# Kernel optimization log

Hardware: AMD Instinct MI355X
Metric: run time of the kernel (lower is better)

The kernel has to match this reference:

```python
import jax, jax.numpy as jnp
import numpy as np

B, S, D, H = 2, 2048, 2048, 16
DH = D // H
CLIP = 8.0
NEG_INF = float('-inf')


def _layernorm(x, g, b, eps=1e-5):
    m = jnp.mean(x, axis=-1, keepdims=True)
    v = jnp.mean(jnp.square(x - m), axis=-1, keepdims=True)
    return (x - m) * jax.lax.rsqrt(v + eps) * g + b


def setup_inputs() -> dict:
    key = jax.random.key(0)
    ks = jax.random.split(key, 6)
    return {
        'x': jax.random.normal(ks[0], (B, S, D), dtype=jnp.float32),
        'attn_bias': jax.random.normal(ks[1], (1, H, 1, S), dtype=jnp.float32) * 0.1,
        'key_padding_mask': jnp.ones((B, S), dtype=bool),
        'Wqkv_w': jax.random.normal(ks[2], (3 * D, D), dtype=jnp.float32) * 0.02,
        'Wqkv_b': jnp.zeros((3 * D,), dtype=jnp.float32),
        'q_ln_g': jnp.ones((D,), dtype=jnp.float32),
        'q_ln_b': jnp.zeros((D,), dtype=jnp.float32),
        'k_ln_g': jnp.ones((D,), dtype=jnp.float32),
        'k_ln_b': jnp.zeros((D,), dtype=jnp.float32),
        'out_w': jax.random.normal(ks[3], (D, D), dtype=jnp.float32) * 0.02,
        'out_b': jnp.zeros((D,), dtype=jnp.float32),
    }


def reference(x, attn_bias, key_padding_mask, Wqkv_w, Wqkv_b,
              q_ln_g, q_ln_b, k_ln_g, k_ln_b, out_w, out_b):
    # Fused QKV projection + clamp
    qkv = x @ Wqkv_w.T + Wqkv_b                      # [B,S,3D]
    qkv = jnp.clip(qkv, -CLIP, CLIP)
    q, k, v = jnp.split(qkv, 3, axis=-1)             # each [B,S,D]
    # Optional per-projection LayerNorm (attn_qk_ln=True)
    q = _layernorm(q, q_ln_g, q_ln_b)
    k = _layernorm(k, k_ln_g, k_ln_b)
    # Split heads
    q = q.reshape(B, S, H, DH)
    k = k.reshape(B, S, H, DH)
    v = v.reshape(B, S, H, DH)
    scale = 1.0 / np.sqrt(DH)
    scores = jnp.einsum('bqhd,bkhd->bhqk', q, k) * scale  # [B,H,S,S]
    scores = scores + attn_bias
    # key padding mask
    scores = jnp.where(key_padding_mask[:, None, None, :], scores, NEG_INF)
    # causal mask
    causal = jnp.tril(jnp.ones((S, S), dtype=bool))
    scores = jnp.where(causal[None, None, :, :], scores, NEG_INF)
    w = jax.nn.softmax(scores, axis=-1)
    ctx = jnp.einsum('bhqk,bkhd->bqhd', w, v).reshape(B, S, D)
    return ctx @ out_w.T + out_b
```

## Files before the change

kernel.cpp:

```cpp
#include <hip/hip_runtime.h>
#include <math.h>

#define B_   2
#define S_   2048
#define D_   2048
#define H_   16
#define DH_  128
#define ND3  6144
#define MROWS 4096

typedef __bf16 bf16;
typedef __attribute__((ext_vector_type(8))) __bf16 bf16x8;
typedef __attribute__((ext_vector_type(4))) float f32x4;

static constexpr float CLIP_V = 8.0f;
static constexpr float SCALE_V = 0.08838834764831845f;

__device__ __forceinline__ void async_load16(const void* g, void* l) {
    __builtin_amdgcn_global_load_lds(
        (const __attribute__((address_space(1))) void*)g,
        (__attribute__((address_space(3))) void*)l, 16, 0, 0);
}

__global__ __launch_bounds__(256) void cvt_kernel(const float* __restrict__ src,
                                                  bf16* __restrict__ dst, int n4)
{
    int i = blockIdx.x * 256 + threadIdx.x;
    if (i >= n4) return;
    float4 v = ((const float4*)src)[i];
    union { bf16 h[4]; uint2 u; } o;
    o.h[0] = (bf16)v.x; o.h[1] = (bf16)v.y; o.h[2] = (bf16)v.z; o.h[3] = (bf16)v.w;
    ((uint2*)dst)[i] = o.u;
}

template <bool CLAMP, typename OUT_T>
__global__ __launch_bounds__(256) void gemm_mfma(
    const bf16* __restrict__ A, const bf16* __restrict__ Bw,
    const float* __restrict__ bias, OUT_T* __restrict__ C,
    int M, int N, int K)
{
    __shared__ __align__(16) bf16 As[128][64];
    __shared__ __align__(16) bf16 Bs[128][64];

    const int tid  = threadIdx.x;
    const int lane = tid & 63;
    const int w    = tid >> 6;
    const int wr   = w >> 1, wc = w & 1;
    const int l15  = lane & 15, lg = lane >> 4;
    const int m0 = blockIdx.y * 128, n0 = blockIdx.x * 128;

    f32x4 acc[4][4] = {};

    const int srow = lane >> 3;
    const int scol = (lane & 7) * 8;

    for (int k0 = 0; k0 < K; k0 += 64) {
#pragma unroll
        for (int c = 0; c < 4; ++c) {
            int r = (c * 4 + w) * 8 + srow;
            async_load16(A  + (size_t)(m0 + r) * K + k0 + scol,
                         (char*)&As[0][0] + (c * 4 + w) * 1024);
            async_load16(Bw + (size_t)(n0 + r) * K + k0 + scol,
                         (char*)&Bs[0][0] + (c * 4 + w) * 1024);
        }
        __syncthreads();

#pragma unroll
        for (int kk = 0; kk < 2; ++kk) {
            bf16x8 af[4], bfv[4];
#pragma unroll
            for (int i = 0; i < 4; ++i) {
                int ra = wr * 64 + i * 16 + l15;
                af[i]  = *(const bf16x8*)((const char*)&As[0][0] + ra * 128 + kk * 64 + lg * 16);
                int rb = wc * 64 + i * 16 + l15;
                bfv[i] = *(const bf16x8*)((const char*)&Bs[0][0] + rb * 128 + kk * 64 + lg * 16);
            }
#pragma unroll
            for (int i = 0; i < 4; ++i)
#pragma unroll
                for (int j = 0; j < 4; ++j)
                    acc[i][j] = __builtin_amdgcn_mfma_f32_16x16x32_bf16(
                        af[i], bfv[j], acc[i][j], 0, 0, 0);
        }
        __syncthreads();
    }

#pragma unroll
    for (int j = 0; j < 4; ++j) {
        int n = n0 + wc * 64 + j * 16 + l15;
        float bn = bias[n];
#pragma unroll
        for (int i = 0; i < 4; ++i) {
            int mbase = m0 + wr * 64 + i * 16 + lg * 4;
#pragma unroll
            for (int r = 0; r < 4; ++r) {
                float v = acc[i][j][r] + bn;
                if (CLAMP) v = fminf(fmaxf(v, -CLIP_V), CLIP_V);
                if constexpr (sizeof(OUT_T) == 2)
                    C[(size_t)(mbase + r) * N + n] = (OUT_T)v;
                else
                    C[(size_t)(mbase + r) * N + n] = v;
            }
        }
    }
}

__global__ __launch_bounds__(256) void ln_kernel(
    bf16* __restrict__ qkv,
    const float* __restrict__ g_q, const float* __restrict__ b_q,
    const float* __restrict__ g_k, const float* __restrict__ b_k)
{
    const int row = blockIdx.x, part = blockIdx.y;
    bf16* p = qkv + (size_t)row * ND3 + part * D_;
    const float* g  = part ? g_k : g_q;
    const float* bb = part ? b_k : b_q;
    const int tid = threadIdx.x;

    union { uint4 u; bf16 h[8]; } in;
    in.u = *(const uint4*)(p + tid * 8);
    float v[8], s = 0.f, ss = 0.f;
#pragma unroll
    for (int i = 0; i < 8; ++i) { v[i] = (float)in.h[i]; s += v[i]; ss += v[i] * v[i]; }

#pragma unroll
    for (int off = 32; off >= 1; off >>= 1) {
        s  += __shfl_down(s, off);
        ss += __shfl_down(ss, off);
    }
    __shared__ float red[2][4];
    const int wid = tid >> 6;
    if ((tid & 63) == 0) { red[0][wid] = s; red[1][wid] = ss; }
    __syncthreads();
    s  = red[0][0] + red[0][1] + red[0][2] + red[0][3];
    ss = red[1][0] + red[1][1] + red[1][2] + red[1][3];

    const float mean = s * (1.0f / (float)D_);
    const float var  = ss * (1.0f / (float)D_) - mean * mean;
    const float inv  = rsqrtf(var + 1e-5f);

    float4 g0 = *(const float4*)(g  + tid * 8);
    float4 g1 = *(const float4*)(g  + tid * 8 + 4);
    float4 c0 = *(const float4*)(bb + tid * 8);
    float4 c1 = *(const float4*)(bb + tid * 8 + 4);
    float gg[8] = {g0.x, g0.y, g0.z, g0.w, g1.x, g1.y, g1.z, g1.w};
    float cc[8] = {c0.x, c0.y, c0.z, c0.w, c1.x, c1.y, c1.z, c1.w};
    union { uint4 u; bf16 h[8]; } o;
#pragma unroll
    for (int i = 0; i < 8; ++i)
        o.h[i] = (bf16)((v[i] - mean) * inv * gg[i] + cc[i]);
    *(uint4*)(p + tid * 8) = o.u;
}

__global__ __launch_bounds__(256) void vtrans_kernel(
    const bf16* __restrict__ qkv, bf16* __restrict__ vT)
{
    __shared__ bf16 T[64][76];
    const int s0 = blockIdx.x * 64, d0 = blockIdx.y * 64, b = blockIdx.z;
    const int tid = threadIdx.x;

#pragma unroll
    for (int l = 0; l < 2; ++l) {
        int idx = tid + l * 256;
        int r = idx >> 3, c = idx & 7;
        const bf16* src = qkv + (size_t)(b * S_ + s0 + r) * ND3 + 2 * D_ + d0 + c * 8;
        uint2 u0 = *(const uint2*)src;
        uint2 u1 = *(const uint2*)(src + 4);
        *(uint2*)((char*)&T[0][0] + r * 152 + c * 16)     = u0;
        *(uint2*)((char*)&T[0][0] + r * 152 + c * 16 + 8) = u1;
    }
    __syncthreads();
#pragma unroll
    for (int l = 0; l < 2; ++l) {
        int idx = tid + l * 256;
        int rd = idx >> 3, cs = idx & 7;
        int d = d0 + rd;
        union { uint4 u; bf16 h[8]; } o;
#pragma unroll
        for (int j = 0; j < 8; ++j) o.h[j] = T[cs * 8 + j][rd];
        int h = d >> 7, dh = d & 127;
        *(uint4*)(vT + (size_t)((b * H_ + h) * DH_ + dh) * S_ + s0 + cs * 8) = o.u;
    }
}

__global__ __launch_bounds__(256) void attn_kernel(
    const bf16* __restrict__ qkv, const bf16* __restrict__ vT,
    const float* __restrict__ attn_bias, bf16* __restrict__ ctx)
{
    __shared__ __align__(16) bf16 Ks[64][128];
    __shared__ __align__(16) bf16 Vt[128][64];
    __shared__ __align__(16) bf16 Ps[4][16][72];

    const int qt  = (gridDim.x - 1) - blockIdx.x;
    const int bh  = blockIdx.y;
    const int b   = bh >> 4, h = bh & 15;
    const int tid = threadIdx.x;
    const int lane = tid & 63;
    const int w    = tid >> 6;
    const int l15  = lane & 15, lg = lane >> 4;
    const int q0   = qt * 64;
    const int qrow = q0 + w * 16 + l15;

    const bf16* qbase  = qkv + (size_t)b * S_ * ND3;
    const bf16* qhead  = qbase + h * DH_;
    const bf16* khead  = qbase + D_ + h * DH_;
    const bf16* vslice = vT + (size_t)(b * H_ + h) * DH_ * S_;
    const float* biasrow = attn_bias + h * S_;

    bf16x8 qf[4];
#pragma unroll
    for (int c = 0; c < 4; ++c)
        qf[c] = *(const bf16x8*)(qhead + (size_t)qrow * ND3 + c * 32 + lg * 8);

    float m_run = -INFINITY, l_run = 0.f;
    f32x4 o[8] = {};

    const int nt = qt + 1;
    for (int kt = 0; kt < nt; ++kt) {
        const int k0 = kt * 64;
#pragma unroll
        for (int c = 0; c < 4; ++c) {
            int rk = (c * 4 + w) * 4 + lg;
            async_load16(khead + (size_t)(k0 + rk) * ND3 + l15 * 8,
                         (char*)&Ks[0][0] + (c * 4 + w) * 1024);
            int rd = (c * 4 + w) * 8 + (lane >> 3);
            async_load16(vslice + (size_t)rd * S_ + k0 + (lane & 7) * 8,
                         (char*)&Vt[0][0] + (c * 4 + w) * 1024);
        }
        __syncthreads();

        f32x4 st[4];
#pragma unroll
        for (int kb = 0; kb < 4; ++kb) {
            f32x4 a = {0.f, 0.f, 0.f, 0.f};
#pragma unroll
            for (int c = 0; c < 4; ++c) {
                bf16x8 kf = *(const bf16x8*)((const char*)&Ks[0][0] +
                               (kb * 16 + l15) * 256 + c * 64 + lg * 16);
                a = __builtin_amdgcn_mfma_f32_16x16x32_bf16(kf, qf[c], a, 0, 0, 0);
            }
            st[kb] = a;
        }

        const bool diag = (kt == qt);
        float vals[4][4];
        float tmax = -INFINITY;
#pragma unroll
        for (int kb = 0; kb < 4; ++kb) {
            float4 b4 = *(const float4*)(biasrow + k0 + kb * 16 + lg * 4);
            float bbv[4] = {b4.x, b4.y, b4.z, b4.w};
#pragma unroll
            for (int r = 0; r < 4; ++r) {
                int key = k0 + kb * 16 + lg * 4 + r;
                float v = st[kb][r] * SCALE_V + bbv[r];
                if (diag && key > qrow) v = -INFINITY;
                vals[kb][r] = v;
                tmax = fmaxf(tmax, v);
            }
        }
        tmax = fmaxf(tmax, __shfl_xor(tmax, 16));
        tmax = fmaxf(tmax, __shfl_xor(tmax, 32));
        float m_new = fmaxf(m_run, tmax);
        float corr  = __expf(m_run - m_new);
        float rsum = 0.f;
#pragma unroll
        for (int kb = 0; kb < 4; ++kb) {
            union { bf16 hh[4]; uint2 u; } pk;
#pragma unroll
            for (int r = 0; r < 4; ++r) {
                float p = __expf(vals[kb][r] - m_new);
                rsum += p;
                pk.hh[r] = (bf16)p;
            }
            *(uint2*)((char*)&Ps[w][0][0] + l15 * 144 + kb * 32 + lg * 8) = pk.u;
        }
        rsum += __shfl_xor(rsum, 16);
        rsum += __shfl_xor(rsum, 32);
        l_run = l_run * corr + rsum;
        m_run = m_new;

        float c0 = __shfl(corr, lg * 4 + 0);
        float c1 = __shfl(corr, lg * 4 + 1);
        float c2 = __shfl(corr, lg * 4 + 2);
        float c3 = __shfl(corr, lg * 4 + 3);
#pragma unroll
        for (int d = 0; d < 8; ++d) {
            o[d][0] *= c0; o[d][1] *= c1; o[d][2] *= c2; o[d][3] *= c3;
        }

        bf16x8 pa0 = *(const bf16x8*)((const char*)&Ps[w][0][0] + l15 * 144 + lg * 16);
        bf16x8 pa1 = *(const bf16x8*)((const char*)&Ps[w][0][0] + l15 * 144 + 64 + lg * 16);
#pragma unroll
        for (int d = 0; d < 8; ++d) {
            bf16x8 vb0 = *(const bf16x8*)((const char*)&Vt[0][0] + (d * 16 + l15) * 128 + lg * 16);
            bf16x8 vb1 = *(const bf16x8*)((const char*)&Vt[0][0] + (d * 16 + l15) * 128 + 64 + lg * 16);
            o[d] = __builtin_amdgcn_mfma_f32_16x16x32_bf16(pa0, vb0, o[d], 0, 0, 0);
            o[d] = __builtin_amdgcn_mfma_f32_16x16x32_bf16(pa1, vb1, o[d], 0, 0, 0);
        }
        __syncthreads();
    }

    float linv = 1.0f / l_run;
    float f0 = __shfl(linv, lg * 4 + 0);
    float f1 = __shfl(linv, lg * 4 + 1);
    float f2 = __shfl(linv, lg * 4 + 2);
    float f3 = __shfl(linv, lg * 4 + 3);
    const int qb = q0 + w * 16 + lg * 4;
#pragma unroll
    for (int d = 0; d < 8; ++d) {
        int dcol = h * DH_ + d * 16 + l15;
        ctx[(size_t)(b * S_ + qb + 0) * D_ + dcol] = (bf16)(o[d][0] * f0);
        ctx[(size_t)(b * S_ + qb + 1) * D_ + dcol] = (bf16)(o[d][1] * f1);
        ctx[(size_t)(b * S_ + qb + 2) * D_ + dcol] = (bf16)(o[d][2] * f2);
        ctx[(size_t)(b * S_ + qb + 3) * D_ + dcol] = (bf16)(o[d][3] * f3);
    }
}

extern "C" void kernel_launch(void* const* d_in, const int* in_sizes, int n_in,
                              void* d_out, int out_size, void* d_ws, size_t ws_size,
                              hipStream_t stream)
{
    const float* x      = (const float*)d_in[0];
    const float* attn_b = (const float*)d_in[1];
    const float* Wqkv_w = (const float*)d_in[3];
    const float* Wqkv_b = (const float*)d_in[4];
    const float* q_ln_g = (const float*)d_in[5];
    const float* q_ln_b = (const float*)d_in[6];
    const float* k_ln_g = (const float*)d_in[7];
    const float* k_ln_b = (const float*)d_in[8];
    const float* out_w  = (const float*)d_in[9];
    const float* out_b  = (const float*)d_in[10];
    float* out = (float*)d_out;

    char* base = (char*)d_ws;
    bf16* xb   = (bf16*)(base);
    bf16* vTb  = (bf16*)(base);
    bf16* wb   = (bf16*)(base + 16777216);
    bf16* ctxb = (bf16*)(base + 16777216);
    bf16* owb  = (bf16*)(base + 41943040);
    bf16* qkvb = (bf16*)(base + 50331648);

    dim3 blk(256);

    cvt_kernel<<<dim3((MROWS * D_ / 4) / 256), blk, 0, stream>>>(x, xb, MROWS * D_ / 4);
    cvt_kernel<<<dim3((ND3 * D_ / 4) / 256), blk, 0, stream>>>(Wqkv_w, wb, ND3 * D_ / 4);
    cvt_kernel<<<dim3((D_ * D_ / 4) / 256), blk, 0, stream>>>(out_w, owb, D_ * D_ / 4);

    gemm_mfma<true, bf16><<<dim3(ND3 / 128, MROWS / 128), blk, 0, stream>>>(
        xb, wb, Wqkv_b, qkvb, MROWS, ND3, D_);

    ln_kernel<<<dim3(MROWS, 2), blk, 0, stream>>>(qkvb, q_ln_g, q_ln_b, k_ln_g, k_ln_b);

    vtrans_kernel<<<dim3(S_ / 64, D_ / 64, B_), blk, 0, stream>>>(qkvb, vTb);

    attn_kernel<<<dim3(S_ / 64, B_ * H_), blk, 0, stream>>>(qkvb, vTb, attn_b, ctxb);

    gemm_mfma<false, float><<<dim3(D_ / 128, MROWS / 128), blk, 0, stream>>>(
        ctxb, owb, out_b, out, MROWS, D_, D_);
}
```

Measured before the change: 608.5 us.

## Pair causal query tiles per block and XOR-swizzle K/V shared memory

Each attention block now handles two query tiles, a high tile (31-p) and a low tile (p), so every block does the same amount of causal work. The K/V tiles it loads are shared by both query tiles, which cuts global K/V traffic. The K and V shared-memory layouts are XOR-swizzled on load and read to reduce LDS bank conflicts. In exchange the grid is halved to 512 blocks, which may lower occupancy and wave count, and holding two sets of accumulators and Q fragments raises register pressure.

Result: faster. 499.2 us (-18.0%).

```diff
diff --git a/kernel.cpp b/kernel.cpp
--- a/kernel.cpp
+++ b/kernel.cpp
@@ -182,6 +182,85 @@
     }
 }
 
+__device__ __forceinline__ void attn_step(
+    const bf16x8 (&qf)[4], float& m_run, float& l_run, f32x4 (&o)[8],
+    int qrow, bool diag, int k0,
+    const char* KsB, const char* VtB, char* PsW,
+    const float* biasrow, int l15, int lg)
+{
+    f32x4 st[4];
+#pragma unroll
+    for (int kb = 0; kb < 4; ++kb) {
+        f32x4 a = {0.f, 0.f, 0.f, 0.f};
+        int r = kb * 16 + l15;
+#pragma unroll
+        for (int c = 0; c < 4; ++c) {
+            int slot = (c * 4 + lg) ^ (r & 7);
+            bf16x8 kf = *(const bf16x8*)(KsB + r * 256 + slot * 16);
+            a = __builtin_amdgcn_mfma_f32_16x16x32_bf16(kf, qf[c], a, 0, 0, 0);
+        }
+        st[kb] = a;
+    }
+
+    float vals[4][4];
+    float tmax = -INFINITY;
+#pragma unroll
+    for (int kb = 0; kb < 4; ++kb) {
+        float4 b4 = *(const float4*)(biasrow + k0 + kb * 16 + lg * 4);
+        float bbv[4] = {b4.x, b4.y, b4.z, b4.w};
+#pragma unroll
+        for (int r = 0; r < 4; ++r) {
+            int key = k0 + kb * 16 + lg * 4 + r;
+            float v = st[kb][r] * SCALE_V + bbv[r];
+            if (diag && key > qrow) v = -INFINITY;
+            vals[kb][r] = v;
+            tmax = fmaxf(tmax, v);
+        }
+    }
+    tmax = fmaxf(tmax, __shfl_xor(tmax, 16));
+    tmax = fmaxf(tmax, __shfl_xor(tmax, 32));
+    float m_new = fmaxf(m_run, tmax);
+    float corr  = __expf(m_run - m_new);
+    float rsum = 0.f;
+#pragma unroll
+    for (int kb = 0; kb < 4; ++kb) {
+        union { bf16 hh[4]; uint2 u; } pk;
+#pragma unroll
+        for (int r = 0; r < 4; ++r) {
+            float pv = __expf(vals[kb][r] - m_new);
+            rsum += pv;
+            pk.hh[r] = (bf16)pv;
+        }
+        *(uint2*)(PsW + l15 * 144 + kb * 32 + lg * 8) = pk.u;
+    }
+    rsum += __shfl_xor(rsum, 16);
+    rsum += __shfl_xor(rsum, 32);
+    l_run = l_run * corr + rsum;
+    m_run = m_new;
+
+    float c0 = __shfl(corr, lg * 4 + 0);
+    float c1 = __shfl(corr, lg * 4 + 1);
+    float c2 = __shfl(corr, lg * 4 + 2);
+    float c3 = __shfl(corr, lg * 4 + 3);
+#pragma unroll
+    for (int d = 0; d < 8; ++d) {
+        o[d][0] *= c0; o[d][1] *= c1; o[d][2] *= c2; o[d][3] *= c3;
+    }
+
+    bf16x8 pa0 = *(const bf16x8*)(PsW + l15 * 144 + lg * 16);
+    bf16x8 pa1 = *(const bf16x8*)(PsW + l15 * 144 + 64 + lg * 16);
+#pragma unroll
+    for (int d = 0; d < 8; ++d) {
+        int r = d * 16 + l15;
+        int s0v = lg ^ (r & 7);
+        int s1v = (lg + 4) ^ (r & 7);
+        bf16x8 vb0 = *(const bf16x8*)(VtB + r * 128 + s0v * 16);
+        bf16x8 vb1 = *(const bf16x8*)(VtB + r * 128 + s1v * 16);
+        o[d] = __builtin_amdgcn_mfma_f32_16x16x32_bf16(pa0, vb0, o[d], 0, 0, 0);
+        o[d] = __builtin_amdgcn_mfma_f32_16x16x32_bf16(pa1, vb1, o[d], 0, 0, 0);
+    }
+}
+
 __global__ __launch_bounds__(256) void attn_kernel(
     const bf16* __restrict__ qkv, const bf16* __restrict__ vT,
     const float* __restrict__ attn_bias, bf16* __restrict__ ctx)
@@ -190,15 +269,16 @@
     __shared__ __align__(16) bf16 Vt[128][64];
     __shared__ __align__(16) bf16 Ps[4][16][72];
 
-    const int qt  = (gridDim.x - 1) - blockIdx.x;
+    const int p   = blockIdx.x;
+    const int qtH = 31 - p, qtL = p;
     const int bh  = blockIdx.y;
     const int b   = bh >> 4, h = bh & 15;
     const int tid = threadIdx.x;
     const int lane = tid & 63;
     const int w    = tid >> 6;
     const int l15  = lane & 15, lg = lane >> 4;
-    const int q0   = qt * 64;
-    const int qrow = q0 + w * 16 + l15;
+    const int qrowH = qtH * 64 + w * 16 + l15;
+    const int qrowL = qtL * 64 + w * 16 + l15;
 
     const bf16* qbase  = qkv + (size_t)b * S_ * ND3;
     const bf16* qhead  = qbase + h * DH_;
@@ -206,112 +286,58 @@
     const bf16* vslice = vT + (size_t)(b * H_ + h) * DH_ * S_;
     const float* biasrow = attn_bias + h * S_;
 
-    bf16x8 qf[4];
-#pragma unroll
-    for (int c = 0; c < 4; ++c)
-        qf[c] = *(const bf16x8*)(qhead + (size_t)qrow * ND3 + c * 32 + lg * 8);
-
-    float m_run = -INFINITY, l_run = 0.f;
-    f32x4 o[8] = {};
-
-    const int nt = qt + 1;
+    const char* KsB = (const char*)&Ks[0][0];
+    const char* VtB = (const char*)&Vt[0][0];
+    char* PsW = (char*)&Ps[w][0][0];
+
+    bf16x8 qfH[4], qfL[4];
+#pragma unroll
+    for (int c = 0; c < 4; ++c) {
+        qfH[c] = *(const bf16x8*)(qhead + (size_t)qrowH * ND3 + c * 32 + lg * 8);
+        qfL[c] = *(const bf16x8*)(qhead + (size_t)qrowL * ND3 + c * 32 + lg * 8);
+    }
+
+    float mH = -INFINITY, lH = 0.f, mL = -INFINITY, lL = 0.f;
+    f32x4 oH[8] = {}, oL[8] = {};
+
+    const int nt = qtH + 1;
     for (int kt = 0; kt < nt; ++kt) {
         const int k0 = kt * 64;
 #pragma unroll
         for (int c = 0; c < 4; ++c) {
             int rk = (c * 4 + w) * 4 + lg;
-            async_load16(khead + (size_t)(k0 + rk) * ND3 + l15 * 8,
+            async_load16(khead + (size_t)(k0 + rk) * ND3 + (l15 ^ (rk & 7)) * 8,
                          (char*)&Ks[0][0] + (c * 4 + w) * 1024);
             int rd = (c * 4 + w) * 8 + (lane >> 3);
-            async_load16(vslice + (size_t)rd * S_ + k0 + (lane & 7) * 8,
+            async_load16(vslice + (size_t)rd * S_ + k0 + ((lane & 7) ^ (rd & 7)) * 8,
                          (char*)&Vt[0][0] + (c * 4 + w) * 1024);
         }
         __syncthreads();
 
-        f32x4 st[4];
-#pragma unroll
-        for (int kb = 0; kb < 4; ++kb) {
-            f32x4 a = {0.f, 0.f, 0.f, 0.f};
-#pragma unroll
-            for (int c = 0; c < 4; ++c) {
-                bf16x8 kf = *(const bf16x8*)((const char*)&Ks[0][0] +
-                               (kb * 16 + l15) * 256 + c * 64 + lg * 16);
-                a = __builtin_amdgcn_mfma_f32_16x16x32_bf16(kf, qf[c], a, 0, 0, 0);
-            }
-            st[kb] = a;
-        }
-
-        const bool diag = (kt == qt);
-        float vals[4][4];
-        float tmax = -INFINITY;
-#pragma unroll
-        for (int kb = 0; kb < 4; ++kb) {
-            float4 b4 = *(const float4*)(biasrow + k0 + kb * 16 + lg * 4);
-            float bbv[4] = {b4.x, b4.y, b4.z, b4.w};
-#pragma unroll
-            for (int r = 0; r < 4; ++r) {
-                int key = k0 + kb * 16 + lg * 4 + r;
-                float v = st[kb][r] * SCALE_V + bbv[r];
-                if (diag && key > qrow) v = -INFINITY;
-                vals[kb][r] = v;
-                tmax = fmaxf(tmax, v);
-            }
-        }
-        tmax = fmaxf(tmax, __shfl_xor(tmax, 16));
-        tmax = fmaxf(tmax, __shfl_xor(tmax, 32));
-        float m_new = fmaxf(m_run, tmax);
-        float corr  = __expf(m_run - m_new);
-        float rsum = 0.f;
-#pragma unroll
-        for (int kb = 0; kb < 4; ++kb) {
-            union { bf16 hh[4]; uint2 u; } pk;
-#pragma unroll
-            for (int r = 0; r < 4; ++r) {
-                float p = __expf(vals[kb][r] - m_new);
-                rsum += p;
-                pk.hh[r] = (bf16)p;
-            }
-            *(uint2*)((char*)&Ps[w][0][0] + l15 * 144 + kb * 32 + lg * 8) = pk.u;
-        }
-        rsum += __shfl_xor(rsum, 16);
-        rsum += __shfl_xor(rsum, 32);
-        l_run = l_run * corr + rsum;
-        m_run = m_new;
-
-        float c0 = __shfl(corr, lg * 4 + 0);
-        float c1 = __shfl(corr, lg * 4 + 1);
-        float c2 = __shfl(corr, lg * 4 + 2);
-        float c3 = __shfl(corr, lg * 4 + 3);
+        attn_step(qfH, mH, lH, oH, qrowH, kt == qtH, k0, KsB, VtB, PsW, biasrow, l15, lg);
+        if (kt <= qtL)
+            attn_step(qfL, mL, lL, oL, qrowL, kt == qtL, k0, KsB, VtB, PsW, biasrow, l15, lg);
+
+        __syncthreads();
+    }
+
+#pragma unroll
+    for (int t = 0; t < 2; ++t) {
+        float linv = 1.0f / (t == 0 ? lH : lL);
+        float f0 = __shfl(linv, lg * 4 + 0);
+        float f1 = __shfl(linv, lg * 4 + 1);
+        float f2 = __shfl(linv, lg * 4 + 2);
+        float f3 = __shfl(linv, lg * 4 + 3);
+        const int qb = (t == 0 ? qtH : qtL) * 64 + w * 16 + lg * 4;
 #pragma unroll
         for (int d = 0; d < 8; ++d) {
-            o[d][0] *= c0; o[d][1] *= c1; o[d][2] *= c2; o[d][3] *= c3;
-        }
-
-        bf16x8 pa0 = *(const bf16x8*)((const char*)&Ps[w][0][0] + l15 * 144 + lg * 16);
-        bf16x8 pa1 = *(const bf16x8*)((const char*)&Ps[w][0][0] + l15 * 144 + 64 + lg * 16);
-#pragma unroll
-        for (int d = 0; d < 8; ++d) {
-            bf16x8 vb0 = *(const bf16x8*)((const char*)&Vt[0][0] + (d * 16 + l15) * 128 + lg * 16);
-            bf16x8 vb1 = *(const bf16x8*)((const char*)&Vt[0][0] + (d * 16 + l15) * 128 + 64 + lg * 16);
-            o[d] = __builtin_amdgcn_mfma_f32_16x16x32_bf16(pa0, vb0, o[d], 0, 0, 0);
-            o[d] = __builtin_amdgcn_mfma_f32_16x16x32_bf16(pa1, vb1, o[d], 0, 0, 0);
-        }
-        __syncthreads();
-    }
-
-    float linv = 1.0f / l_run;
-    float f0 = __shfl(linv, lg * 4 + 0);
-    float f1 = __shfl(linv, lg * 4 + 1);
-    float f2 = __shfl(linv, lg * 4 + 2);
-    float f3 = __shfl(linv, lg * 4 + 3);
-    const int qb = q0 + w * 16 + lg * 4;
-#pragma unroll
-    for (int d = 0; d < 8; ++d) {
-        int dcol = h * DH_ + d * 16 + l15;
-        ctx[(size_t)(b * S_ + qb + 0) * D_ + dcol] = (bf16)(o[d][0] * f0);
-        ctx[(size_t)(b * S_ + qb + 1) * D_ + dcol] = (bf16)(o[d][1] * f1);
-        ctx[(size_t)(b * S_ + qb + 2) * D_ + dcol] = (bf16)(o[d][2] * f2);
-        ctx[(size_t)(b * S_ + qb + 3) * D_ + dcol] = (bf16)(o[d][3] * f3);
+            f32x4 ov = (t == 0) ? oH[d] : oL[d];
+            int dcol = h * DH_ + d * 16 + l15;
+            ctx[(size_t)(b * S_ + qb + 0) * D_ + dcol] = (bf16)(ov[0] * f0);
+            ctx[(size_t)(b * S_ + qb + 1) * D_ + dcol] = (bf16)(ov[1] * f1);
+            ctx[(size_t)(b * S_ + qb + 2) * D_ + dcol] = (bf16)(ov[2] * f2);
+            ctx[(size_t)(b * S_ + qb + 3) * D_ + dcol] = (bf16)(ov[3] * f3);
+        }
     }
 }
 
@@ -352,7 +378,7 @@
 
     vtrans_kernel<<<dim3(S_ / 64, D_ / 64, B_), blk, 0, stream>>>(qkvb, vTb);
 
-    attn_kernel<<<dim3(S_ / 64, B_ * H_), blk, 0, stream>>>(qkvb, vTb, attn_b, ctxb);
+    attn_kernel<<<dim3(16, B_ * H_), blk, 0, stream>>>(qkvb, vTb, attn_b, ctxb);
 
     gemm_mfma<false, float><<<dim3(D_ / 128, MROWS / 128), blk, 0, stream>>>(
         ctxb, owb, out_b, out, MROWS, D_, D_);
```
